# Kernel tuning notes

Hardware: AMD Instinct MI355X
Metric: run time of the kernel (lower is better)

The kernel has to match this reference:

```python
import jax, jax.numpy as jnp
import numpy as np

B, N, T, K = 128, 64, 512, 5
FS = 120.0  # sampling rate implied by rfftfreq(N, d=1/120) in FFT_for_Period


def setup_inputs() -> dict:
    key = jax.random.key(0)
    x = jax.random.normal(key, (B, N, T), dtype=jnp.float32)
    return {"x": x}


def _gather_time(S, ix):
    # S: [B, T2, N]; ix: [B, K, T] int indices along time axis -> [B, K, T, N]
    b = ix.shape[0]
    g = jnp.take_along_axis(S, ix.reshape(b, -1)[:, :, None], axis=1)
    return g.reshape(ix.shape + (S.shape[-1],))


def _fft_trend(x, k_top=K):
    # Faithful vectorization of FFT_TREND.forward: x [B, N, T] -> trends [B, N, K, T]
    xt = jnp.transpose(x, (0, 2, 1))  # [B, T, N]
    Tn = xt.shape[1]
    # FFT_for_Period: mean |rfft| over nodes, zero DC bin, top-k frequency bins
    mag = jnp.abs(jnp.fft.rfft(xt, axis=1)).mean(-1)  # [B, F]
    mag = mag.at[:, 0].set(0.0)
    _, top_idx = jax.lax.top_k(mag, k_top)  # [B, K]
    freqs = jnp.fft.rfftfreq(Tn, d=1.0 / FS).astype(jnp.float32)
    scale = jnp.floor(Tn / freqs[top_idx]).astype(jnp.int32)  # top_scale = T // top_freq, [B, K]
    # static bound: smallest nonzero freq is FS/T -> max kernel = T*T/FS
    pmax = (Tn * Tn) // int(FS)
    scale = jnp.clip(scale, 1, pmax)
    pad = (pmax - 1) // 2 + 1
    # edge-replicated extension (matches moving_avg front/end repeat padding)
    idx = jnp.clip(jnp.arange(-pad, Tn + pad), 0, Tn - 1)
    ext = xt[:, idx, :]  # [B, T + 2*pad, N]
    S = jnp.concatenate([jnp.zeros_like(ext[:, :1]), jnp.cumsum(ext, axis=1)], axis=1)
    t = jnp.arange(Tn)
    k = scale[:, :, None]                      # [B, K, 1] data-dependent kernel sizes
    p = (k - 1) // 2                           # moving_avg pad = (k-1)//2 per side
    L = Tn + 2 * p - k + 1                     # AvgPool1d output length (T odd-k, T-1 even-k)
    tc = jnp.minimum(t[None, None, :], L - 1)  # repeat-last-row fix for even kernels
    start = tc - p + pad                       # [B, K, T] window starts in ext coords
    win = _gather_time(S, start + k) - _gather_time(S, start)  # [B, K, T, N] window sums
    mean = win / k[..., None].astype(xt.dtype)                  # moving averages
    # torch: stack over K -> [K,B,T,N], permute(1,3,0,2) -> [B,N,K,T]
    return jnp.transpose(mean, (0, 3, 1, 2))


def reference(x):
    return _fft_trend(x)
```

## Files before the change

kernel.cpp:

```cpp
#include <hip/hip_runtime.h>
#include <cmath>

namespace {

constexpr int B_ = 128;
constexpr int N_ = 64;
constexpr int T_ = 512;
constexpr int K_ = 5;
constexpr int NBINS = 257;
constexpr int PMAX = 2184;
constexpr int ROWS = 4;
constexpr int FROWS = 8;
constexpr int CHUNKS = N_ / FROWS;

struct cpx { float re, im; };
__device__ __forceinline__ cpx cadd(cpx a, cpx b) { return {a.re + b.re, a.im + b.im}; }
__device__ __forceinline__ cpx csub(cpx a, cpx b) { return {a.re - b.re, a.im - b.im}; }
__device__ __forceinline__ cpx cmul(cpx a, cpx b) {
  return {a.re * b.re - a.im * b.im, a.re * b.im + a.im * b.re};
}

__device__ __forceinline__ void radix8(
    cpx z0, cpx z1, cpx z2, cpx z3, cpx z4, cpx z5, cpx z6, cpx z7,
    cpx& t0, cpx& t1, cpx& t2, cpx& t3, cpx& t4, cpx& t5, cpx& t6, cpx& t7) {
  const float c = 0.70710678118654752f;
  cpx a0 = cadd(z0, z4), a1 = csub(z0, z4);
  cpx a2 = cadd(z2, z6), a3 = csub(z2, z6);
  cpx a4 = cadd(z1, z5), a5 = csub(z1, z5);
  cpx a6 = cadd(z3, z7), a7 = csub(z3, z7);
  cpx b0 = cadd(a0, a2), b1 = csub(a0, a2);
  cpx b2 = cadd(a4, a6), b3 = csub(a4, a6);
  t0 = cadd(b0, b2);
  t4 = csub(b0, b2);
  t2 = {b1.re + b3.im, b1.im - b3.re};
  t6 = {b1.re - b3.im, b1.im + b3.re};
  cpx ua5  = {c * (a5.re + a5.im), c * (a5.im - a5.re)};
  cpx usa5 = {c * (a5.re - a5.im), c * (a5.re + a5.im)};
  cpx ua7  = {c * (a7.re + a7.im), c * (a7.im - a7.re)};
  cpx usa7 = {c * (a7.re - a7.im), c * (a7.re + a7.im)};
  cpx mia3 = {a3.im, -a3.re};
  cpx pia3 = {-a3.im, a3.re};
  t1 = cadd(cadd(a1, ua5), csub(mia3, usa7));
  t3 = cadd(csub(a1, usa5), cadd(pia3, ua7));
  t5 = cadd(csub(a1, ua5), cadd(mia3, usa7));
  t7 = cadd(cadd(a1, usa5), csub(pia3, ua7));
}

__device__ __forceinline__ void p1_row(const float* __restrict__ src, int j,
                                       cpx wj, float* __restrict__ br,
                                       float* __restrict__ bi) {
  const float x0v = src[j], x1v = src[j + 64], x2v = src[j + 128], x3v = src[j + 192];
  const float x4v = src[j + 256], x5v = src[j + 320], x6v = src[j + 384], x7v = src[j + 448];
  const float c = 0.70710678118654752f;
  const float s04 = x0v + x4v, d04 = x0v - x4v;
  const float s26 = x2v + x6v, d26 = x2v - x6v;
  const float s15 = x1v + x5v, d15 = x1v - x5v;
  const float s37 = x3v + x7v, d37 = x3v - x7v;
  const float se = s04 + s26, so = s15 + s37;
  const float cm = c * (d15 - d37), cp = c * (d15 + d37);
  const cpx y0 = {se + so, 0.f};
  const cpx y1 = {d04 + cm, -(d26 + cp)};
  const cpx y2 = {s04 - s26, s37 - s15};
  const cpx y3 = {d04 - cm, d26 - cp};
  const cpx y4 = {se - so, 0.f};
  const cpx y5 = {d04 - cm, cp - d26};
  const cpx y6 = {s04 - s26, s15 - s37};
  const cpx y7 = {d04 + cm, d26 + cp};
  const int p = j * 9;
  cpx tw = wj, z;
  br[p + 0] = y0.re;              bi[p + 0] = y0.im;
  z = cmul(y1, tw); br[p + 1] = z.re; bi[p + 1] = z.im; tw = cmul(tw, wj);
  z = cmul(y2, tw); br[p + 2] = z.re; bi[p + 2] = z.im; tw = cmul(tw, wj);
  z = cmul(y3, tw); br[p + 3] = z.re; bi[p + 3] = z.im; tw = cmul(tw, wj);
  z = cmul(y4, tw); br[p + 4] = z.re; bi[p + 4] = z.im; tw = cmul(tw, wj);
  z = cmul(y5, tw); br[p + 5] = z.re; bi[p + 5] = z.im; tw = cmul(tw, wj);
  z = cmul(y6, tw); br[p + 6] = z.re; bi[p + 6] = z.im; tw = cmul(tw, wj);
  z = cmul(y7, tw); br[p + 7] = z.re; bi[p + 7] = z.im;
}

__device__ __forceinline__ void p2_row(int r2, int i2, cpx wi,
                                       float* __restrict__ br,
                                       float* __restrict__ bi) {
  const int p = i2 * 9 + r2;
  const cpx zz0 = {br[p +   0], bi[p +   0]};
  const cpx zz1 = {br[p +  72], bi[p +  72]};
  const cpx zz2 = {br[p + 144], bi[p + 144]};
  const cpx zz3 = {br[p + 216], bi[p + 216]};
  const cpx zz4 = {br[p + 288], bi[p + 288]};
  const cpx zz5 = {br[p + 360], bi[p + 360]};
  const cpx zz6 = {br[p + 432], bi[p + 432]};
  const cpx zz7 = {br[p + 504], bi[p + 504]};
  cpx t0, t1, t2, t3, t4, t5, t6, t7;
  radix8(zz0, zz1, zz2, zz3, zz4, zz5, zz6, zz7, t0, t1, t2, t3, t4, t5, t6, t7);
  cpx tw = wi;
  cpx y1 = cmul(t1, tw); tw = cmul(tw, wi);
  cpx y2 = cmul(t2, tw); tw = cmul(tw, wi);
  cpx y3 = cmul(t3, tw); tw = cmul(tw, wi);
  cpx y4 = cmul(t4, tw); tw = cmul(tw, wi);
  cpx y5 = cmul(t5, tw); tw = cmul(tw, wi);
  cpx y6 = cmul(t6, tw); tw = cmul(tw, wi);
  cpx y7 = cmul(t7, tw);
  const int q = r2 * 72 + i2;
  br[q +  0] = t0.re; bi[q +  0] = t0.im;
  br[q +  9] = y1.re; bi[q +  9] = y1.im;
  br[q + 18] = y2.re; bi[q + 18] = y2.im;
  br[q + 27] = y3.re; bi[q + 27] = y3.im;
  br[q + 36] = y4.re; bi[q + 36] = y4.im;
  br[q + 45] = y5.re; bi[q + 45] = y5.im;
  br[q + 54] = y6.re; bi[q + 54] = y6.im;
  br[q + 63] = y7.re; bi[q + 63] = y7.im;
}

__device__ __forceinline__ void p3_row(int r3, int c3,
                                       const float* __restrict__ br,
                                       const float* __restrict__ bi,
                                       float& m0, float& m1, float& m2,
                                       float& m3, float& m4) {
  const int p = r3 * 72 + c3 * 9;
  const cpx yy0 = {br[p + 0], bi[p + 0]};
  const cpx yy1 = {br[p + 1], bi[p + 1]};
  const cpx yy2 = {br[p + 2], bi[p + 2]};
  const cpx yy3 = {br[p + 3], bi[p + 3]};
  const cpx yy4 = {br[p + 4], bi[p + 4]};
  const cpx yy5 = {br[p + 5], bi[p + 5]};
  const cpx yy6 = {br[p + 6], bi[p + 6]};
  const cpx yy7 = {br[p + 7], bi[p + 7]};
  cpx X0, X1, X2, X3, X4, X5, X6, X7;
  radix8(yy0, yy1, yy2, yy3, yy4, yy5, yy6, yy7, X0, X1, X2, X3, X4, X5, X6, X7);
  m0 = sqrtf(X0.re * X0.re + X0.im * X0.im);
  m1 = sqrtf(X1.re * X1.re + X1.im * X1.im);
  m2 = sqrtf(X2.re * X2.re + X2.im * X2.im);
  m3 = sqrtf(X3.re * X3.re + X3.im * X3.im);
  m4 = sqrtf(X4.re * X4.re + X4.im * X4.im);
}

__global__ __launch_bounds__(256, 4) void fft_mag_kernel(const float* __restrict__ x,
                                                         float* __restrict__ magp) {
  const int tid = threadIdx.x;
  const int w = tid >> 6;
  const int lane = tid & 63;
  const int rowA = blockIdx.x * FROWS + 2 * w;

  __shared__ float bre[FROWS][576];
  __shared__ float bim[FROWS][576];

  float* brA = &bre[2 * w][0];
  float* biA = &bim[2 * w][0];
  float* brB = &bre[2 * w + 1][0];
  float* biB = &bim[2 * w + 1][0];

  const float* srcA = x + ((size_t)rowA << 9);
  const float* srcB = srcA + T_;

  {
    float sj, cj;
    __sincosf((float)lane * 0.01227184630308513f , &sj, &cj);
    const cpx wj = {cj, -sj};
    p1_row(srcA, lane, wj, brA, biA);
    p1_row(srcB, lane, wj, brB, biB);
  }

  const int r2 = lane >> 3, i2 = lane & 7;
  {
    float si, ci;
    __sincosf((float)i2 * 0.09817477042468103f , &si, &ci);
    const cpx wi = {ci, -si};
    p2_row(r2, i2, wi, brA, biA);
    p2_row(r2, i2, wi, brB, biB);
  }

  {
    float a0, a1, a2, a3, a4, b0, b1, b2, b3, b4;
    p3_row(r2, i2, brA, biA, a0, a1, a2, a3, a4);
    p3_row(r2, i2, brB, biB, b0, b1, b2, b3, b4);
    const int kb = (i2 << 3) + r2;
    brA[kb +   0] = a0 + b0;
    brA[kb +  64] = a1 + b1;
    brA[kb + 128] = a2 + b2;
    brA[kb + 192] = a3 + b3;
    if (kb == 0) brA[256] = a4 + b4;
  }
  __syncthreads();

  for (int bin = tid; bin < NBINS; bin += 256) {
    magp[(size_t)blockIdx.x * NBINS + bin] =
        bre[0][bin] + bre[2][bin] + bre[4][bin] + bre[6][bin];
  }
}

__global__ __launch_bounds__(256) void trend_topk_kernel(const float* __restrict__ x,
                                                         const float* __restrict__ magp,
                                                         float* __restrict__ out) {
  const int tid = threadIdx.x;
  const int w = tid >> 6;
  const int lane = tid & 63;
  const int bn = blockIdx.x * ROWS + w;
  const int b = bn >> 6;

  __shared__ float m[NBINS];
  __shared__ int sc[K_];
  __shared__ double P[ROWS][T_ + 1];

  for (int i = tid; i < NBINS; i += 256) {
    float s = -1.0f;
    if (i != 0) {
      s = 0.0f;
      const float* mp = magp + (size_t)b * CHUNKS * NBINS + i;
#pragma unroll
      for (int c = 0; c < CHUNKS; ++c) s += mp[c * NBINS];
    }
    m[i] = s;
  }
  __syncthreads();

  if (w == 0) {
    float q0 = m[lane], q1 = m[lane + 64], q2 = m[lane + 128], q3 = m[lane + 192];
    float q4 = (lane == 0) ? m[256] : -1.0e30f;
    const int i0 = lane, i1 = lane + 64, i2x = lane + 128, i3 = lane + 192;
    const int i4 = (lane == 0) ? 256 : NBINS + 1;
#pragma unroll
    for (int kk = 0; kk < K_; ++kk) {
      float bv = q0; int bi = i0;
      if (q1 > bv) { bv = q1; bi = i1; }
      if (q2 > bv) { bv = q2; bi = i2x; }
      if (q3 > bv) { bv = q3; bi = i3; }
      if (q4 > bv) { bv = q4; bi = i4; }
      for (int off = 32; off > 0; off >>= 1) {
        const float ov = __shfl_down(bv, off);
        const int oi = __shfl_down(bi, off);
        if (ov > bv || (ov == bv && oi < bi)) { bv = ov; bi = oi; }
      }
      bi = __shfl(bi, 0);
      if (lane == 0) {
        int s = 32768 / (15 * bi);
        s = s < 1 ? 1 : (s > PMAX ? PMAX : s);
        sc[kk] = s;
      }
      if (bi == i0) q0 = -1.0e30f;
      else if (bi == i1) q1 = -1.0e30f;
      else if (bi == i2x) q2 = -1.0e30f;
      else if (bi == i3) q3 = -1.0e30f;
      else if (bi == i4) q4 = -1.0e30f;
    }
  }

  const float* src = x + ((size_t)bn << 9);
  const float4 v0 = *reinterpret_cast<const float4*>(src + (lane << 3));
  const float4 v1 = *reinterpret_cast<const float4*>(src + (lane << 3) + 4);

  double e0 = (double)v0.x;
  double e1 = e0 + (double)v0.y;
  double e2 = e1 + (double)v0.z;
  double e3 = e2 + (double)v0.w;
  double e4 = e3 + (double)v1.x;
  double e5 = e4 + (double)v1.y;
  double e6 = e5 + (double)v1.z;
  double e7 = e6 + (double)v1.w;

  double v = e7;
  for (int off = 1; off < 64; off <<= 1) {
    const double o = __shfl_up(v, off);
    if (lane >= off) v += o;
  }
  const double base = v - e7;

  double* Pw = P[w];
  if (lane == 0) Pw[0] = 0.0;
  const int p0 = (lane << 3) + 1;
  Pw[p0 + 0] = base + e0;
  Pw[p0 + 1] = base + e1;
  Pw[p0 + 2] = base + e2;
  Pw[p0 + 3] = base + e3;
  Pw[p0 + 4] = base + e4;
  Pw[p0 + 5] = base + e5;
  Pw[p0 + 6] = base + e6;
  Pw[p0 + 7] = base + e7;
  __syncthreads();

  const double x0 = Pw[1];
  const double xl = Pw[T_] - Pw[T_ - 1];

  float* outbn = out + (((size_t)bn * K_) << 9);
#pragma unroll
  for (int kk = 0; kk < K_; ++kk) {
    const int k = sc[kk];
    const int p = (k - 1) >> 1;
    const int Lm1 = T_ + 2 * p - k;
    const double invk = 1.0 / (double)k;
#pragma unroll
    for (int u = 0; u < 8; ++u) {
      const int t = lane + (u << 6);
      const int tc = t < Lm1 ? t : Lm1;
      const int lo = tc - p;
      const int hi = lo + k;
      const int cl = lo < 0 ? -lo : 0;
      const int cr = hi > T_ ? hi - T_ : 0;
      const int loc = lo < 0 ? 0 : lo;
      const int hic = hi > T_ ? T_ : hi;
      const double sum = Pw[hic] - Pw[loc] + (double)cl * x0 + (double)cr * xl;
      outbn[(kk << 9) + t] = (float)(sum * invk);
    }
  }
}

}

extern "C" void kernel_launch(void* const* d_in, const int* in_sizes, int n_in,
                              void* d_out, int out_size, void* d_ws, size_t ws_size,
                              hipStream_t stream) {
  const float* x = (const float*)d_in[0];
  float* out = (float*)d_out;

  float* magp = (float*)d_ws;

  hipLaunchKernelGGL(fft_mag_kernel, dim3(B_ * N_ / FROWS), dim3(256), 0, stream, x, magp);
  hipLaunchKernelGGL(trend_topk_kernel, dim3(B_ * N_ / ROWS), dim3(256), 0, stream, x, magp, out);
}
```

Measured before the change: 38.03 us.

## Pack two real rows into one complex FFT and use float prefix sums

The FFT magnitude kernel now treats two real input rows as the real and imaginary parts of a single 512-point complex FFT per wave. It separates their spectra with the conjugate-symmetry identity, which roughly halves the FFT butterfly work and the shared memory per block; explicit scheduling barriers replace the implicit ordering the old helpers gave. The trend kernel switches its prefix-sum scan, shared buffer and window averages from double to float, cutting FP64 arithmetic and halving the LDS footprint. The cost is reduced accuracy in the cumulative sums over 512 samples, and a small extra unpacking step per bin.

```diff
diff --git a/kernel.cpp b/kernel.cpp
--- a/kernel.cpp
+++ b/kernel.cpp
@@ -46,92 +46,8 @@
   t7 = cadd(cadd(a1, usa5), csub(pia3, ua7));
 }
 
-__device__ __forceinline__ void p1_row(const float* __restrict__ src, int j,
-                                       cpx wj, float* __restrict__ br,
-                                       float* __restrict__ bi) {
-  const float x0v = src[j], x1v = src[j + 64], x2v = src[j + 128], x3v = src[j + 192];
-  const float x4v = src[j + 256], x5v = src[j + 320], x6v = src[j + 384], x7v = src[j + 448];
-  const float c = 0.70710678118654752f;
-  const float s04 = x0v + x4v, d04 = x0v - x4v;
-  const float s26 = x2v + x6v, d26 = x2v - x6v;
-  const float s15 = x1v + x5v, d15 = x1v - x5v;
-  const float s37 = x3v + x7v, d37 = x3v - x7v;
-  const float se = s04 + s26, so = s15 + s37;
-  const float cm = c * (d15 - d37), cp = c * (d15 + d37);
-  const cpx y0 = {se + so, 0.f};
-  const cpx y1 = {d04 + cm, -(d26 + cp)};
-  const cpx y2 = {s04 - s26, s37 - s15};
-  const cpx y3 = {d04 - cm, d26 - cp};
-  const cpx y4 = {se - so, 0.f};
-  const cpx y5 = {d04 - cm, cp - d26};
-  const cpx y6 = {s04 - s26, s15 - s37};
-  const cpx y7 = {d04 + cm, d26 + cp};
-  const int p = j * 9;
-  cpx tw = wj, z;
-  br[p + 0] = y0.re;              bi[p + 0] = y0.im;
-  z = cmul(y1, tw); br[p + 1] = z.re; bi[p + 1] = z.im; tw = cmul(tw, wj);
-  z = cmul(y2, tw); br[p + 2] = z.re; bi[p + 2] = z.im; tw = cmul(tw, wj);
-  z = cmul(y3, tw); br[p + 3] = z.re; bi[p + 3] = z.im; tw = cmul(tw, wj);
-  z = cmul(y4, tw); br[p + 4] = z.re; bi[p + 4] = z.im; tw = cmul(tw, wj);
-  z = cmul(y5, tw); br[p + 5] = z.re; bi[p + 5] = z.im; tw = cmul(tw, wj);
-  z = cmul(y6, tw); br[p + 6] = z.re; bi[p + 6] = z.im; tw = cmul(tw, wj);
-  z = cmul(y7, tw); br[p + 7] = z.re; bi[p + 7] = z.im;
-}
-
-__device__ __forceinline__ void p2_row(int r2, int i2, cpx wi,
-                                       float* __restrict__ br,
-                                       float* __restrict__ bi) {
-  const int p = i2 * 9 + r2;
-  const cpx zz0 = {br[p +   0], bi[p +   0]};
-  const cpx zz1 = {br[p +  72], bi[p +  72]};
-  const cpx zz2 = {br[p + 144], bi[p + 144]};
-  const cpx zz3 = {br[p + 216], bi[p + 216]};
-  const cpx zz4 = {br[p + 288], bi[p + 288]};
-  const cpx zz5 = {br[p + 360], bi[p + 360]};
-  const cpx zz6 = {br[p + 432], bi[p + 432]};
-  const cpx zz7 = {br[p + 504], bi[p + 504]};
-  cpx t0, t1, t2, t3, t4, t5, t6, t7;
-  radix8(zz0, zz1, zz2, zz3, zz4, zz5, zz6, zz7, t0, t1, t2, t3, t4, t5, t6, t7);
-  cpx tw = wi;
-  cpx y1 = cmul(t1, tw); tw = cmul(tw, wi);
-  cpx y2 = cmul(t2, tw); tw = cmul(tw, wi);
-  cpx y3 = cmul(t3, tw); tw = cmul(tw, wi);
-  cpx y4 = cmul(t4, tw); tw = cmul(tw, wi);
-  cpx y5 = cmul(t5, tw); tw = cmul(tw, wi);
-  cpx y6 = cmul(t6, tw); tw = cmul(tw, wi);
-  cpx y7 = cmul(t7, tw);
-  const int q = r2 * 72 + i2;
-  br[q +  0] = t0.re; bi[q +  0] = t0.im;
-  br[q +  9] = y1.re; bi[q +  9] = y1.im;
-  br[q + 18] = y2.re; bi[q + 18] = y2.im;
-  br[q + 27] = y3.re; bi[q + 27] = y3.im;
-  br[q + 36] = y4.re; bi[q + 36] = y4.im;
-  br[q + 45] = y5.re; bi[q + 45] = y5.im;
-  br[q + 54] = y6.re; bi[q + 54] = y6.im;
-  br[q + 63] = y7.re; bi[q + 63] = y7.im;
-}
-
-__device__ __forceinline__ void p3_row(int r3, int c3,
-                                       const float* __restrict__ br,
-                                       const float* __restrict__ bi,
-                                       float& m0, float& m1, float& m2,
-                                       float& m3, float& m4) {
-  const int p = r3 * 72 + c3 * 9;
-  const cpx yy0 = {br[p + 0], bi[p + 0]};
-  const cpx yy1 = {br[p + 1], bi[p + 1]};
-  const cpx yy2 = {br[p + 2], bi[p + 2]};
-  const cpx yy3 = {br[p + 3], bi[p + 3]};
-  const cpx yy4 = {br[p + 4], bi[p + 4]};
-  const cpx yy5 = {br[p + 5], bi[p + 5]};
-  const cpx yy6 = {br[p + 6], bi[p + 6]};
-  const cpx yy7 = {br[p + 7], bi[p + 7]};
-  cpx X0, X1, X2, X3, X4, X5, X6, X7;
-  radix8(yy0, yy1, yy2, yy3, yy4, yy5, yy6, yy7, X0, X1, X2, X3, X4, X5, X6, X7);
-  m0 = sqrtf(X0.re * X0.re + X0.im * X0.im);
-  m1 = sqrtf(X1.re * X1.re + X1.im * X1.im);
-  m2 = sqrtf(X2.re * X2.re + X2.im * X2.im);
-  m3 = sqrtf(X3.re * X3.re + X3.im * X3.im);
-  m4 = sqrtf(X4.re * X4.re + X4.im * X4.im);
+__device__ __forceinline__ void lds_fence() {
+  __builtin_amdgcn_sched_barrier(0);
 }
 
 __global__ __launch_bounds__(256, 4) void fft_mag_kernel(const float* __restrict__ x,
@@ -141,50 +57,149 @@
   const int lane = tid & 63;
   const int rowA = blockIdx.x * FROWS + 2 * w;
 
-  __shared__ float bre[FROWS][576];
-  __shared__ float bim[FROWS][576];
-
-  float* brA = &bre[2 * w][0];
-  float* biA = &bim[2 * w][0];
-  float* brB = &bre[2 * w + 1][0];
-  float* biB = &bim[2 * w + 1][0];
+  __shared__ float bre[4][576];
+  __shared__ float bim[4][576];
+
+  float* br = &bre[w][0];
+  float* bi = &bim[w][0];
 
   const float* srcA = x + ((size_t)rowA << 9);
   const float* srcB = srcA + T_;
 
   {
+    const int j = lane;
+    const cpx z0 = {srcA[j],       srcB[j]};
+    const cpx z1 = {srcA[j +  64], srcB[j +  64]};
+    const cpx z2 = {srcA[j + 128], srcB[j + 128]};
+    const cpx z3 = {srcA[j + 192], srcB[j + 192]};
+    const cpx z4 = {srcA[j + 256], srcB[j + 256]};
+    const cpx z5 = {srcA[j + 320], srcB[j + 320]};
+    const cpx z6 = {srcA[j + 384], srcB[j + 384]};
+    const cpx z7 = {srcA[j + 448], srcB[j + 448]};
+    cpx y0, y1, y2, y3, y4, y5, y6, y7;
+    radix8(z0, z1, z2, z3, z4, z5, z6, z7, y0, y1, y2, y3, y4, y5, y6, y7);
     float sj, cj;
-    __sincosf((float)lane * 0.01227184630308513f , &sj, &cj);
+    __sincosf((float)j * 0.01227184630308513f , &sj, &cj);
     const cpx wj = {cj, -sj};
-    p1_row(srcA, lane, wj, brA, biA);
-    p1_row(srcB, lane, wj, brB, biB);
-  }
+    const int p = j * 9;
+    cpx tw = wj, z;
+    br[p + 0] = y0.re;            bi[p + 0] = y0.im;
+    z = cmul(y1, tw); br[p + 1] = z.re; bi[p + 1] = z.im; tw = cmul(tw, wj);
+    z = cmul(y2, tw); br[p + 2] = z.re; bi[p + 2] = z.im; tw = cmul(tw, wj);
+    z = cmul(y3, tw); br[p + 3] = z.re; bi[p + 3] = z.im; tw = cmul(tw, wj);
+    z = cmul(y4, tw); br[p + 4] = z.re; bi[p + 4] = z.im; tw = cmul(tw, wj);
+    z = cmul(y5, tw); br[p + 5] = z.re; bi[p + 5] = z.im; tw = cmul(tw, wj);
+    z = cmul(y6, tw); br[p + 6] = z.re; bi[p + 6] = z.im; tw = cmul(tw, wj);
+    z = cmul(y7, tw); br[p + 7] = z.re; bi[p + 7] = z.im;
+  }
+  lds_fence();
 
   const int r2 = lane >> 3, i2 = lane & 7;
   {
+    const int p = i2 * 9 + r2;
+    const cpx zz0 = {br[p +   0], bi[p +   0]};
+    const cpx zz1 = {br[p +  72], bi[p +  72]};
+    const cpx zz2 = {br[p + 144], bi[p + 144]};
+    const cpx zz3 = {br[p + 216], bi[p + 216]};
+    const cpx zz4 = {br[p + 288], bi[p + 288]};
+    const cpx zz5 = {br[p + 360], bi[p + 360]};
+    const cpx zz6 = {br[p + 432], bi[p + 432]};
+    const cpx zz7 = {br[p + 504], bi[p + 504]};
+    cpx t0, t1, t2, t3, t4, t5, t6, t7;
+    radix8(zz0, zz1, zz2, zz3, zz4, zz5, zz6, zz7, t0, t1, t2, t3, t4, t5, t6, t7);
     float si, ci;
     __sincosf((float)i2 * 0.09817477042468103f , &si, &ci);
     const cpx wi = {ci, -si};
-    p2_row(r2, i2, wi, brA, biA);
-    p2_row(r2, i2, wi, brB, biB);
-  }
+    cpx tw = wi;
+    cpx y1 = cmul(t1, tw); tw = cmul(tw, wi);
+    cpx y2 = cmul(t2, tw); tw = cmul(tw, wi);
+    cpx y3 = cmul(t3, tw); tw = cmul(tw, wi);
+    cpx y4 = cmul(t4, tw); tw = cmul(tw, wi);
+    cpx y5 = cmul(t5, tw); tw = cmul(tw, wi);
+    cpx y6 = cmul(t6, tw); tw = cmul(tw, wi);
+    cpx y7 = cmul(t7, tw);
+    lds_fence();
+    const int q = r2 * 72 + i2;
+    br[q +  0] = t0.re; bi[q +  0] = t0.im;
+    br[q +  9] = y1.re; bi[q +  9] = y1.im;
+    br[q + 18] = y2.re; bi[q + 18] = y2.im;
+    br[q + 27] = y3.re; bi[q + 27] = y3.im;
+    br[q + 36] = y4.re; bi[q + 36] = y4.im;
+    br[q + 45] = y5.re; bi[q + 45] = y5.im;
+    br[q + 54] = y6.re; bi[q + 54] = y6.im;
+    br[q + 63] = y7.re; bi[q + 63] = y7.im;
+  }
+  lds_fence();
 
   {
-    float a0, a1, a2, a3, a4, b0, b1, b2, b3, b4;
-    p3_row(r2, i2, brA, biA, a0, a1, a2, a3, a4);
-    p3_row(r2, i2, brB, biB, b0, b1, b2, b3, b4);
-    const int kb = (i2 << 3) + r2;
-    brA[kb +   0] = a0 + b0;
-    brA[kb +  64] = a1 + b1;
-    brA[kb + 128] = a2 + b2;
-    brA[kb + 192] = a3 + b3;
-    if (kb == 0) brA[256] = a4 + b4;
+    const int r3 = lane >> 3, c3 = lane & 7;
+    const int p = r3 * 72 + c3 * 9;
+    const cpx yy0 = {br[p + 0], bi[p + 0]};
+    const cpx yy1 = {br[p + 1], bi[p + 1]};
+    const cpx yy2 = {br[p + 2], bi[p + 2]};
+    const cpx yy3 = {br[p + 3], bi[p + 3]};
+    const cpx yy4 = {br[p + 4], bi[p + 4]};
+    const cpx yy5 = {br[p + 5], bi[p + 5]};
+    const cpx yy6 = {br[p + 6], bi[p + 6]};
+    const cpx yy7 = {br[p + 7], bi[p + 7]};
+    cpx X0, X1, X2, X3, X4, X5, X6, X7;
+    radix8(yy0, yy1, yy2, yy3, yy4, yy5, yy6, yy7, X0, X1, X2, X3, X4, X5, X6, X7);
+    lds_fence();
+    const int kb0 = (c3 << 3) + r3;
+    br[kb0 +   0] = X0.re; bi[kb0 +   0] = X0.im;
+    br[kb0 +  64] = X1.re; bi[kb0 +  64] = X1.im;
+    br[kb0 + 128] = X2.re; bi[kb0 + 128] = X2.im;
+    br[kb0 + 192] = X3.re; bi[kb0 + 192] = X3.im;
+    br[kb0 + 256] = X4.re; bi[kb0 + 256] = X4.im;
+    br[kb0 + 320] = X5.re; bi[kb0 + 320] = X5.im;
+    br[kb0 + 384] = X6.re; bi[kb0 + 384] = X6.im;
+    br[kb0 + 448] = X7.re; bi[kb0 + 448] = X7.im;
+  }
+  lds_fence();
+
+  {
+    float m[4];
+    float a0, b0, c0, d0, a1, b1, c1, d1, a2, b2, c2, d2, a3, b3, c3v, d3;
+    {
+      const int k0 = lane, k0m = (512 - k0) & 511;
+      a0 = br[k0]; b0 = bi[k0]; c0 = br[k0m]; d0 = bi[k0m];
+      const int k1 = lane + 64, k1m = 512 - k1;
+      a1 = br[k1]; b1 = bi[k1]; c1 = br[k1m]; d1 = bi[k1m];
+      const int k2 = lane + 128, k2m = 512 - k2;
+      a2 = br[k2]; b2 = bi[k2]; c2 = br[k2m]; d2 = bi[k2m];
+      const int k3 = lane + 192, k3m = 512 - k3;
+      a3 = br[k3]; b3 = bi[k3]; c3v = br[k3m]; d3 = bi[k3m];
+    }
+    float e256r = 0.f, e256i = 0.f;
+    if (lane == 0) { e256r = br[256]; e256i = bi[256]; }
+    lds_fence();
+    {
+      const float sa = a0 + c0, dv = b0 - d0, sv = b0 + d0, du = a0 - c0;
+      m[0] = 0.5f * (sqrtf(sa * sa + dv * dv) + sqrtf(sv * sv + du * du));
+    }
+    {
+      const float sa = a1 + c1, dv = b1 - d1, sv = b1 + d1, du = a1 - c1;
+      m[1] = 0.5f * (sqrtf(sa * sa + dv * dv) + sqrtf(sv * sv + du * du));
+    }
+    {
+      const float sa = a2 + c2, dv = b2 - d2, sv = b2 + d2, du = a2 - c2;
+      m[2] = 0.5f * (sqrtf(sa * sa + dv * dv) + sqrtf(sv * sv + du * du));
+    }
+    {
+      const float sa = a3 + c3v, dv = b3 - d3, sv = b3 + d3, du = a3 - c3v;
+      m[3] = 0.5f * (sqrtf(sa * sa + dv * dv) + sqrtf(sv * sv + du * du));
+    }
+    br[lane]       = m[0];
+    br[lane + 64]  = m[1];
+    br[lane + 128] = m[2];
+    br[lane + 192] = m[3];
+    if (lane == 0) br[256] = fabsf(e256r) + fabsf(e256i);
   }
   __syncthreads();
 
   for (int bin = tid; bin < NBINS; bin += 256) {
     magp[(size_t)blockIdx.x * NBINS + bin] =
-        bre[0][bin] + bre[2][bin] + bre[4][bin] + bre[6][bin];
+        bre[0][bin] + bre[1][bin] + bre[2][bin] + bre[3][bin];
   }
 }
 
@@ -199,7 +214,7 @@
 
   __shared__ float m[NBINS];
   __shared__ int sc[K_];
-  __shared__ double P[ROWS][T_ + 1];
+  __shared__ float P[ROWS][T_ + 1];
 
   for (int i = tid; i < NBINS; i += 256) {
     float s = -1.0f;
@@ -248,24 +263,24 @@
   const float4 v0 = *reinterpret_cast<const float4*>(src + (lane << 3));
   const float4 v1 = *reinterpret_cast<const float4*>(src + (lane << 3) + 4);
 
-  double e0 = (double)v0.x;
-  double e1 = e0 + (double)v0.y;
-  double e2 = e1 + (double)v0.z;
-  double e3 = e2 + (double)v0.w;
-  double e4 = e3 + (double)v1.x;
-  double e5 = e4 + (double)v1.y;
-  double e6 = e5 + (double)v1.z;
-  double e7 = e6 + (double)v1.w;
-
-  double v = e7;
+  float e0 = v0.x;
+  float e1 = e0 + v0.y;
+  float e2 = e1 + v0.z;
+  float e3 = e2 + v0.w;
+  float e4 = e3 + v1.x;
+  float e5 = e4 + v1.y;
+  float e6 = e5 + v1.z;
+  float e7 = e6 + v1.w;
+
+  float v = e7;
   for (int off = 1; off < 64; off <<= 1) {
-    const double o = __shfl_up(v, off);
+    const float o = __shfl_up(v, off);
     if (lane >= off) v += o;
   }
-  const double base = v - e7;
-
-  double* Pw = P[w];
-  if (lane == 0) Pw[0] = 0.0;
+  const float base = v - e7;
+
+  float* Pw = P[w];
+  if (lane == 0) Pw[0] = 0.0f;
   const int p0 = (lane << 3) + 1;
   Pw[p0 + 0] = base + e0;
   Pw[p0 + 1] = base + e1;
@@ -277,8 +292,8 @@
   Pw[p0 + 7] = base + e7;
   __syncthreads();
 
-  const double x0 = Pw[1];
-  const double xl = Pw[T_] - Pw[T_ - 1];
+  const float x0 = Pw[1];
+  const float xl = Pw[T_] - Pw[T_ - 1];
 
   float* outbn = out + (((size_t)bn * K_) << 9);
 #pragma unroll
@@ -286,7 +301,7 @@
     const int k = sc[kk];
     const int p = (k - 1) >> 1;
     const int Lm1 = T_ + 2 * p - k;
-    const double invk = 1.0 / (double)k;
+    const float invk = 1.0f / (float)k;
 #pragma unroll
     for (int u = 0; u < 8; ++u) {
       const int t = lane + (u << 6);
@@ -297,8 +312,8 @@
       const int cr = hi > T_ ? hi - T_ : 0;
       const int loc = lo < 0 ? 0 : lo;
       const int hic = hi > T_ ? T_ : hi;
-      const double sum = Pw[hic] - Pw[loc] + (double)cl * x0 + (double)cr * xl;
-      outbn[(kk << 9) + t] = (float)(sum * invk);
+      const float sum = Pw[hic] - Pw[loc] + (float)cl * x0 + (float)cr * xl;
+      outbn[(kk << 9) + t] = sum * invk;
     }
   }
 }
```

Measured after the change: 32.89 us. 13.5% less time.
